# Performance work log

Hardware: AMD Instinct MI355X
Metric: run time of the kernel (lower is better)

Reference implementation:

```python
import jax, jax.numpy as jnp
import numpy as np

N = 50000
IN_C, HID_C, OUT_C = 128, 256, 128
E = 800000


def sage_conv(x, edge_index, W_l, b_l, W_r, num_nodes):
    # PyG SAGEConv (aggr='mean'): out = lin_l(mean_{j in N(i)} x_j) + lin_r(x_i)
    src, dst = edge_index[0], edge_index[1]
    msgs = x[src]  # [E, C] gather of source features
    agg = jax.ops.segment_sum(msgs, dst, num_segments=num_nodes)  # [N, C]
    deg = jax.ops.segment_sum(jnp.ones((edge_index.shape[1],), x.dtype), dst,
                              num_segments=num_nodes)
    mean = agg / jnp.maximum(deg, 1.0)[:, None]
    return mean @ W_l.T + b_l + x @ W_r.T


def setup_inputs() -> dict:
    key = jax.random.key(0)
    ks = jax.random.split(key, 8)
    x = jax.random.normal(ks[0], (N, IN_C), dtype=jnp.float32)
    edge_index = jax.random.randint(ks[1], (2, E), 0, N, dtype=jnp.int64)
    s1 = 1.0 / np.sqrt(IN_C)
    s2 = 1.0 / np.sqrt(HID_C)
    W1_l = jax.random.uniform(ks[2], (HID_C, IN_C), jnp.float32, -s1, s1)
    W1_r = jax.random.uniform(ks[3], (HID_C, IN_C), jnp.float32, -s1, s1)
    b1 = jnp.zeros((HID_C,), jnp.float32)
    W2_l = jax.random.uniform(ks[4], (OUT_C, HID_C), jnp.float32, -s2, s2)
    W2_r = jax.random.uniform(ks[5], (OUT_C, HID_C), jnp.float32, -s2, s2)
    b2 = jnp.zeros((OUT_C,), jnp.float32)
    return {"x": x, "edge_index": edge_index,
            "W1_l": W1_l, "b1": b1, "W1_r": W1_r,
            "W2_l": W2_l, "b2": b2, "W2_r": W2_r}


def reference(x, edge_index, W1_l, b1, W1_r, W2_l, b2, W2_r):
    h = sage_conv(x, edge_index, W1_l, b1, W1_r, N)
    h = jax.nn.relu(h)
    # dropout p=0.5 is identity in eval mode (inference reference)
    out = sage_conv(h, edge_index, W2_l, b2, W2_r, N)
    return out
```

## Files before the change

kernel.cpp:

```cpp
#include <hip/hip_runtime.h>

#define NN   50000
#define INC  128
#define HIDC 256
#define OUTC 128
#define NE   800000
#define MP   50048
#define CAP  64

#define EPB 4096
#define NCH ((NE + EPB - 1) / EPB)
#define RSZ 6250

typedef short bfrag __attribute__((ext_vector_type(8)));
typedef float f32x4 __attribute__((ext_vector_type(4)));
typedef unsigned short us8 __attribute__((ext_vector_type(8)));

__device__ inline unsigned short f2b(float f) {
    union { float f; unsigned u; } v; v.f = f;
    unsigned u = v.u;
    return (unsigned short)((u + 0x7fffu + ((u >> 16) & 1u)) >> 16);
}
__device__ inline float b2f(unsigned short s) {
    union { unsigned u; float f; } v; v.u = ((unsigned)s) << 16;
    return v.f;
}

__global__ __launch_bounds__(256) void k_prep(
    const float* __restrict__ x, const float* __restrict__ W1l,
    const float* __restrict__ W1r, const float* __restrict__ W2l,
    const float* __restrict__ W2r, unsigned short* __restrict__ xb16,
    unsigned short* __restrict__ A1f, unsigned short* __restrict__ B1f,
    unsigned short* __restrict__ B2f, int* __restrict__ cnt) {
    const int b = blockIdx.x;
    if (b < 3125) {
        int t = b * 256 + threadIdx.x;
        int i = t >> 4;
        int c8 = t & 15;
        const float* src = x + (size_t)i * INC + c8 * 8;
        float4 v0 = *(const float4*)src;
        float4 v1 = *(const float4*)(src + 4);
        us8 o = { f2b(v0.x), f2b(v0.y), f2b(v0.z), f2b(v0.w),
                  f2b(v1.x), f2b(v1.y), f2b(v1.z), f2b(v1.w) };
        *(us8*)(xb16 + (size_t)i * INC + c8 * 8) = o;
        size_t off = (size_t)(i >> 4) * 4096 + (size_t)(4 + (c8 >> 2)) * 512
                   + (size_t)(c8 & 3) * 128 + (size_t)(i & 15) * 8;
        *(us8*)(A1f + off) = o;
    } else if (b < 3157) {
        int t = (b - 3125) * 256 + threadIdx.x;
        int n = t >> 5;
        int k8 = t & 31;
        int k = k8 * 8;
        const float* src = (k < 128) ? (W1l + (size_t)n * INC + k)
                                     : (W1r + (size_t)n * INC + (k - 128));
        float4 v0 = *(const float4*)src;
        float4 v1 = *(const float4*)(src + 4);
        us8 o = { f2b(v0.x), f2b(v0.y), f2b(v0.z), f2b(v0.w),
                  f2b(v1.x), f2b(v1.y), f2b(v1.z), f2b(v1.w) };
        size_t off = (size_t)(n >> 4) * 4096 + (size_t)(k8 >> 2) * 512
                   + (size_t)(k8 & 3) * 128 + (size_t)(n & 15) * 8;
        *(us8*)(B1f + off) = o;
    } else if (b < 3189) {
        int t = (b - 3157) * 256 + threadIdx.x;
        int n = t >> 5;
        int k8 = t & 31;
        const float* src = (n < 128) ? (W2l + (size_t)n * HIDC + k8 * 8)
                                     : (W2r + (size_t)(n - 128) * HIDC + k8 * 8);
        float4 v0 = *(const float4*)src;
        float4 v1 = *(const float4*)(src + 4);
        us8 o = { f2b(v0.x), f2b(v0.y), f2b(v0.z), f2b(v0.w),
                  f2b(v1.x), f2b(v1.y), f2b(v1.z), f2b(v1.w) };
        size_t off = (size_t)(n >> 4) * 4096 + (size_t)(k8 >> 2) * 512
                   + (size_t)(k8 & 3) * 128 + (size_t)(n & 15) * 8;
        *(us8*)(B2f + off) = o;
    } else {
        int t = (b - 3189) * 256 + threadIdx.x;
        if (t < (NN + 3) / 4) *(int4*)(cnt + t * 4) = make_int4(0, 0, 0, 0);
    }
}

__global__ __launch_bounds__(256) void k_fill(const int* __restrict__ ei,
                                              int* __restrict__ cnt,
                                              unsigned short* __restrict__ csr) {
    const int r = blockIdx.x & 7;
    const int c = blockIdx.x >> 3;
    const int lo = r * RSZ, hi = lo + RSZ;
    const int base = c * EPB + threadIdx.x;
#pragma unroll
    for (int i = 0; i < EPB / 256; ++i) {
        int e = base + i * 256;
        if (e < NE) {
            int dst = ei[NE + e];
            if (dst >= lo && dst < hi) {
                int old = atomicAdd(&cnt[dst], 1);
                if (old < CAP) csr[dst * CAP + old] = (unsigned short)ei[e];
            }
        }
    }
}

__global__ __launch_bounds__(256) void k_gather_mean(
    const int* __restrict__ cnt, const unsigned short* __restrict__ csr,
    const unsigned short* __restrict__ xb16, unsigned short* __restrict__ A1f) {
    const int node = blockIdx.x * 4 + (threadIdx.x >> 6);
    const int lane = threadIdx.x & 63;
    const int sub = lane >> 4;
    const int cl = lane & 15;
    const int cn = cnt[node];
    const int m = (cn < CAP) ? cn : CAP;
    const unsigned short* cb = csr + node * CAP;
    float acc[8] = {};
    const unsigned short* xb = xb16 + cl * 8;
    int i = sub;
    for (; i + 4 < m; i += 8) {
        int s0 = cb[i], s1 = cb[i + 4];
        us8 v0 = *(const us8*)(xb + (size_t)s0 * INC);
        us8 v1 = *(const us8*)(xb + (size_t)s1 * INC);
#pragma unroll
        for (int j = 0; j < 8; ++j) acc[j] += b2f(v0[j]) + b2f(v1[j]);
    }
    if (i < m) {
        int s0 = cb[i];
        us8 v0 = *(const us8*)(xb + (size_t)s0 * INC);
#pragma unroll
        for (int j = 0; j < 8; ++j) acc[j] += b2f(v0[j]);
    }
#pragma unroll
    for (int j = 0; j < 8; ++j) {
        acc[j] += __shfl_xor(acc[j], 16, 64);
        acc[j] += __shfl_xor(acc[j], 32, 64);
    }
    if (sub == 0) {
        float inv = 1.0f / fmaxf((float)cn, 1.0f);
        us8 o;
#pragma unroll
        for (int j = 0; j < 8; ++j) o[j] = f2b(acc[j] * inv);
        size_t off = (size_t)(node >> 4) * 4096 + (size_t)(cl >> 2) * 512
                   + (size_t)(cl & 3) * 128 + (size_t)(node & 15) * 8;
        *(us8*)(A1f + off) = o;
    }
}

__global__ __launch_bounds__(256) void k_mgemm1(
    const unsigned short* __restrict__ A, const unsigned short* __restrict__ B,
    const float* __restrict__ bias, unsigned short* __restrict__ H) {
    __shared__ unsigned short Asl[4096];
    __shared__ unsigned short Bsl[4096];
    const int tid = threadIdx.x;
    const int lane = tid & 63;
    const int w = tid >> 6;
    const int wr = w >> 1, wc = w & 1;
    const int col = lane & 15, quad = lane >> 4;
    const int bx = blockIdx.x, by = blockIdx.y;

    f32x4 acc[4][4];
#pragma unroll
    for (int i = 0; i < 4; ++i)
#pragma unroll
        for (int j = 0; j < 4; ++j) acc[i][j] = (f32x4){0.f, 0.f, 0.f, 0.f};

    const int c0 = tid, c1 = tid + 256;
    for (int kc = 0; kc < 8; ++kc) {
        const unsigned short* Ag = A + (size_t)(bx * 8) * 4096 + kc * 512;
        const unsigned short* Bg = B + (size_t)(by * 8) * 4096 + kc * 512;
        __syncthreads();
        *(us8*)(Asl + c0 * 8) = *(const us8*)(Ag + (size_t)(c0 >> 6) * 4096 + (c0 & 63) * 8);
        *(us8*)(Asl + c1 * 8) = *(const us8*)(Ag + (size_t)(c1 >> 6) * 4096 + (c1 & 63) * 8);
        *(us8*)(Bsl + c0 * 8) = *(const us8*)(Bg + (size_t)(c0 >> 6) * 4096 + (c0 & 63) * 8);
        *(us8*)(Bsl + c1 * 8) = *(const us8*)(Bg + (size_t)(c1 >> 6) * 4096 + (c1 & 63) * 8);
        __syncthreads();
        bfrag a[4], b[4];
#pragma unroll
        for (int mt = 0; mt < 4; ++mt)
            a[mt] = *(const bfrag*)(Asl + (wr * 4 + mt) * 512 + quad * 128 + col * 8);
#pragma unroll
        for (int nt = 0; nt < 4; ++nt)
            b[nt] = *(const bfrag*)(Bsl + (wc * 4 + nt) * 512 + quad * 128 + col * 8);
#pragma unroll
        for (int mt = 0; mt < 4; ++mt)
#pragma unroll
            for (int nt = 0; nt < 4; ++nt)
                acc[mt][nt] = __builtin_amdgcn_mfma_f32_16x16x32_bf16(a[mt], b[nt], acc[mt][nt], 0, 0, 0);
    }
#pragma unroll
    for (int mt = 0; mt < 4; ++mt)
#pragma unroll
        for (int nt = 0; nt < 4; ++nt) {
            int n = by * 128 + wc * 64 + nt * 16 + col;
            float bb = bias[n];
#pragma unroll
            for (int r = 0; r < 4; ++r) {
                int m = bx * 128 + wr * 64 + mt * 16 + quad * 4 + r;
                if (m < NN) {
                    size_t off = (size_t)(m >> 4) * 4096 + (size_t)(n >> 5) * 512
                               + (size_t)((n >> 3) & 3) * 128 + (size_t)(m & 15) * 8 + (n & 7);
                    H[off] = f2b(fmaxf(acc[mt][nt][r] + bb, 0.f));
                }
            }
        }
}

__global__ __launch_bounds__(256) void k_mgemm2(
    const unsigned short* __restrict__ A, const unsigned short* __restrict__ B,
    const float* __restrict__ bias, unsigned short* __restrict__ HP,
    float* __restrict__ OUT) {
    __shared__ unsigned short Asl[4096];
    __shared__ unsigned short Bsl[4096];
    const int tid = threadIdx.x;
    const int lane = tid & 63;
    const int w = tid >> 6;
    const int wr = w >> 1, wc = w & 1;
    const int col = lane & 15, quad = lane >> 4;
    const int bx = blockIdx.x, by = blockIdx.y;

    f32x4 acc[4][4];
#pragma unroll
    for (int i = 0; i < 4; ++i)
#pragma unroll
        for (int j = 0; j < 4; ++j) acc[i][j] = (f32x4){0.f, 0.f, 0.f, 0.f};

    const int c0 = tid, c1 = tid + 256;
    for (int kc = 0; kc < 8; ++kc) {
        const unsigned short* Ag = A + (size_t)(bx * 8) * 4096 + kc * 512;
        const unsigned short* Bg = B + (size_t)(by * 8) * 4096 + kc * 512;
        __syncthreads();
        *(us8*)(Asl + c0 * 8) = *(const us8*)(Ag + (size_t)(c0 >> 6) * 4096 + (c0 & 63) * 8);
        *(us8*)(Asl + c1 * 8) = *(const us8*)(Ag + (size_t)(c1 >> 6) * 4096 + (c1 & 63) * 8);
        *(us8*)(Bsl + c0 * 8) = *(const us8*)(Bg + (size_t)(c0 >> 6) * 4096 + (c0 & 63) * 8);
        *(us8*)(Bsl + c1 * 8) = *(const us8*)(Bg + (size_t)(c1 >> 6) * 4096 + (c1 & 63) * 8);
        __syncthreads();
        bfrag a[4], b[4];
#pragma unroll
        for (int mt = 0; mt < 4; ++mt)
            a[mt] = *(const bfrag*)(Asl + (wr * 4 + mt) * 512 + quad * 128 + col * 8);
#pragma unroll
        for (int nt = 0; nt < 4; ++nt)
            b[nt] = *(const bfrag*)(Bsl + (wc * 4 + nt) * 512 + quad * 128 + col * 8);
#pragma unroll
        for (int mt = 0; mt < 4; ++mt)
#pragma unroll
            for (int nt = 0; nt < 4; ++nt)
                acc[mt][nt] = __builtin_amdgcn_mfma_f32_16x16x32_bf16(a[mt], b[nt], acc[mt][nt], 0, 0, 0);
    }
    if (by == 0) {
#pragma unroll
        for (int mt = 0; mt < 4; ++mt)
#pragma unroll
            for (int nt = 0; nt < 4; ++nt) {
                int n = wc * 64 + nt * 16 + col;
#pragma unroll
                for (int r = 0; r < 4; ++r) {
                    int m = bx * 128 + wr * 64 + mt * 16 + quad * 4 + r;
                    if (m < NN) HP[(size_t)m * OUTC + n] = f2b(acc[mt][nt][r]);
                }
            }
    } else {
#pragma unroll
        for (int mt = 0; mt < 4; ++mt)
#pragma unroll
            for (int nt = 0; nt < 4; ++nt) {
                int n = wc * 64 + nt * 16 + col;
                float bb = bias[n];
#pragma unroll
                for (int r = 0; r < 4; ++r) {
                    int m = bx * 128 + wr * 64 + mt * 16 + quad * 4 + r;
                    if (m < NN) OUT[(size_t)m * OUTC + n] = acc[mt][nt][r] + bb;
                }
            }
    }
}

__global__ __launch_bounds__(256) void k_gather_add(
    const int* __restrict__ cnt, const unsigned short* __restrict__ csr,
    const unsigned short* __restrict__ hp, float* __restrict__ out) {
    const int node = blockIdx.x * 4 + (threadIdx.x >> 6);
    const int lane = threadIdx.x & 63;
    const int sub = lane >> 4;
    const int cl = lane & 15;
    const int cn = cnt[node];
    const int m = (cn < CAP) ? cn : CAP;
    const unsigned short* cb = csr + node * CAP;
    float acc[8] = {};
    const unsigned short* hb = hp + cl * 8;
    int i = sub;
    for (; i + 4 < m; i += 8) {
        int s0 = cb[i], s1 = cb[i + 4];
        us8 v0 = *(const us8*)(hb + (size_t)s0 * OUTC);
        us8 v1 = *(const us8*)(hb + (size_t)s1 * OUTC);
#pragma unroll
        for (int j = 0; j < 8; ++j) acc[j] += b2f(v0[j]) + b2f(v1[j]);
    }
    if (i < m) {
        int s0 = cb[i];
        us8 v0 = *(const us8*)(hb + (size_t)s0 * OUTC);
#pragma unroll
        for (int j = 0; j < 8; ++j) acc[j] += b2f(v0[j]);
    }
#pragma unroll
    for (int j = 0; j < 8; ++j) {
        acc[j] += __shfl_xor(acc[j], 16, 64);
        acc[j] += __shfl_xor(acc[j], 32, 64);
    }
    if (sub == 0) {
        float inv = 1.0f / fmaxf((float)cn, 1.0f);
        float* p = out + (size_t)node * OUTC + cl * 8;
        float4 c0v = *(float4*)p;
        float4 c1v = *(float4*)(p + 4);
        c0v.x += acc[0] * inv; c0v.y += acc[1] * inv;
        c0v.z += acc[2] * inv; c0v.w += acc[3] * inv;
        c1v.x += acc[4] * inv; c1v.y += acc[5] * inv;
        c1v.z += acc[6] * inv; c1v.w += acc[7] * inv;
        *(float4*)p = c0v;
        *(float4*)(p + 4) = c1v;
    }
}

extern "C" void kernel_launch(void* const* d_in, const int* in_sizes, int n_in,
                              void* d_out, int out_size, void* d_ws, size_t ws_size,
                              hipStream_t stream) {
    const float* x   = (const float*)d_in[0];
    const int*   ei  = (const int*)d_in[1];
    const float* W1l = (const float*)d_in[2];
    const float* b1  = (const float*)d_in[3];
    const float* W1r = (const float*)d_in[4];
    const float* W2l = (const float*)d_in[5];
    const float* b2  = (const float*)d_in[6];
    const float* W2r = (const float*)d_in[7];
    float* out = (float*)d_out;

    int* cnt = (int*)d_ws;
    unsigned short* csr = (unsigned short*)(cnt + ((NN + 63) & ~63));
    unsigned short* A1f  = csr + (size_t)NN * CAP;
    unsigned short* Hf   = A1f + (size_t)MP * 256;
    unsigned short* xb16 = Hf + (size_t)MP * 256;
    unsigned short* hp   = xb16 + (size_t)NN * 128;
    unsigned short* B1f  = hp + (size_t)NN * 128;
    unsigned short* B2f  = B1f + 256 * 256;

    k_prep<<<3238, 256, 0, stream>>>(x, W1l, W1r, W2l, W2r, xb16, A1f, B1f, B2f, cnt);
    k_fill<<<NCH * 8, 256, 0, stream>>>(ei, cnt, csr);
    k_gather_mean<<<NN / 4, 256, 0, stream>>>(cnt, csr, xb16, A1f);

    dim3 g(MP / 128, 2);
    k_mgemm1<<<g, 256, 0, stream>>>(A1f, B1f, b1, Hf);
    k_mgemm2<<<g, 256, 0, stream>>>(Hf, B2f, b2, hp, out);

    k_gather_add<<<NN / 4, 256, 0, stream>>>(cnt, csr, hp, out);
}
```

Baseline: 247.3 us.

## Fuse the two dense GEMMs into one kernel keeping hidden tile in LDS

Merges the layer-1 GEMM (with bias and ReLU) and the layer-2 GEMM into a single kernel. Each block loads a 64-row A tile into shared memory once, writes the hidden activations back into the same LDS buffer, and runs the second GEMM from there. This removes the global round trip of the 50k x 256 hidden matrix and one kernel launch. B fragments are now read directly from global memory rather than staged through LDS, and there are fewer, larger blocks using 32KB of LDS each, which may lower occupancy.

New measurement: 227.9 us. 7.9% less time.

```diff
diff --git a/kernel.cpp b/kernel.cpp
--- a/kernel.cpp
+++ b/kernel.cpp
@@ -141,116 +141,93 @@
     }
 }
 
-__global__ __launch_bounds__(256) void k_mgemm1(
-    const unsigned short* __restrict__ A, const unsigned short* __restrict__ B,
-    const float* __restrict__ bias, unsigned short* __restrict__ H) {
-    __shared__ unsigned short Asl[4096];
-    __shared__ unsigned short Bsl[4096];
+__global__ __launch_bounds__(256) void k_mgemm_fused(
+    const unsigned short* __restrict__ A, const unsigned short* __restrict__ B1,
+    const float* __restrict__ b1, const unsigned short* __restrict__ B2,
+    const float* __restrict__ b2, unsigned short* __restrict__ HP,
+    float* __restrict__ OUT) {
+    __shared__ unsigned short Hsl[16384];
     const int tid = threadIdx.x;
     const int lane = tid & 63;
     const int w = tid >> 6;
-    const int wr = w >> 1, wc = w & 1;
     const int col = lane & 15, quad = lane >> 4;
-    const int bx = blockIdx.x, by = blockIdx.y;
+    const int m0 = blockIdx.x * 64;
+
+    {
+        const us8* src = (const us8*)(A + (size_t)(m0 >> 4) * 4096);
+        us8* dst = (us8*)Hsl;
+#pragma unroll
+        for (int i = 0; i < 8; ++i) dst[tid + i * 256] = src[tid + i * 256];
+    }
+    __syncthreads();
 
     f32x4 acc[4][4];
 #pragma unroll
     for (int i = 0; i < 4; ++i)
 #pragma unroll
         for (int j = 0; j < 4; ++j) acc[i][j] = (f32x4){0.f, 0.f, 0.f, 0.f};
-
-    const int c0 = tid, c1 = tid + 256;
+#pragma unroll
     for (int kc = 0; kc < 8; ++kc) {
-        const unsigned short* Ag = A + (size_t)(bx * 8) * 4096 + kc * 512;
-        const unsigned short* Bg = B + (size_t)(by * 8) * 4096 + kc * 512;
-        __syncthreads();
-        *(us8*)(Asl + c0 * 8) = *(const us8*)(Ag + (size_t)(c0 >> 6) * 4096 + (c0 & 63) * 8);
-        *(us8*)(Asl + c1 * 8) = *(const us8*)(Ag + (size_t)(c1 >> 6) * 4096 + (c1 & 63) * 8);
-        *(us8*)(Bsl + c0 * 8) = *(const us8*)(Bg + (size_t)(c0 >> 6) * 4096 + (c0 & 63) * 8);
-        *(us8*)(Bsl + c1 * 8) = *(const us8*)(Bg + (size_t)(c1 >> 6) * 4096 + (c1 & 63) * 8);
-        __syncthreads();
         bfrag a[4], b[4];
 #pragma unroll
         for (int mt = 0; mt < 4; ++mt)
-            a[mt] = *(const bfrag*)(Asl + (wr * 4 + mt) * 512 + quad * 128 + col * 8);
+            a[mt] = *(const bfrag*)(Hsl + mt * 4096 + kc * 512 + quad * 128 + col * 8);
 #pragma unroll
         for (int nt = 0; nt < 4; ++nt)
-            b[nt] = *(const bfrag*)(Bsl + (wc * 4 + nt) * 512 + quad * 128 + col * 8);
+            b[nt] = *(const bfrag*)(B1 + (size_t)(w * 4 + nt) * 4096 + kc * 512 + quad * 128 + col * 8);
 #pragma unroll
         for (int mt = 0; mt < 4; ++mt)
 #pragma unroll
             for (int nt = 0; nt < 4; ++nt)
                 acc[mt][nt] = __builtin_amdgcn_mfma_f32_16x16x32_bf16(a[mt], b[nt], acc[mt][nt], 0, 0, 0);
     }
-#pragma unroll
-    for (int mt = 0; mt < 4; ++mt)
-#pragma unroll
-        for (int nt = 0; nt < 4; ++nt) {
-            int n = by * 128 + wc * 64 + nt * 16 + col;
-            float bb = bias[n];
+    __syncthreads();
+
+#pragma unroll
+    for (int nt = 0; nt < 4; ++nt) {
+        int n = w * 64 + nt * 16 + col;
+        float bb = b1[n];
+        int noff = (n >> 5) * 512 + ((n >> 3) & 3) * 128 + (n & 7);
+#pragma unroll
+        for (int mt = 0; mt < 4; ++mt) {
 #pragma unroll
             for (int r = 0; r < 4; ++r) {
-                int m = bx * 128 + wr * 64 + mt * 16 + quad * 4 + r;
-                if (m < NN) {
-                    size_t off = (size_t)(m >> 4) * 4096 + (size_t)(n >> 5) * 512
-                               + (size_t)((n >> 3) & 3) * 128 + (size_t)(m & 15) * 8 + (n & 7);
-                    H[off] = f2b(fmaxf(acc[mt][nt][r] + bb, 0.f));
-                }
+                int ml = quad * 4 + r;
+                Hsl[mt * 4096 + noff + ml * 8] = f2b(fmaxf(acc[mt][nt][r] + bb, 0.f));
             }
         }
-}
-
-__global__ __launch_bounds__(256) void k_mgemm2(
-    const unsigned short* __restrict__ A, const unsigned short* __restrict__ B,
-    const float* __restrict__ bias, unsigned short* __restrict__ HP,
-    float* __restrict__ OUT) {
-    __shared__ unsigned short Asl[4096];
-    __shared__ unsigned short Bsl[4096];
-    const int tid = threadIdx.x;
-    const int lane = tid & 63;
-    const int w = tid >> 6;
-    const int wr = w >> 1, wc = w & 1;
-    const int col = lane & 15, quad = lane >> 4;
-    const int bx = blockIdx.x, by = blockIdx.y;
-
-    f32x4 acc[4][4];
+    }
+    __syncthreads();
+
 #pragma unroll
     for (int i = 0; i < 4; ++i)
 #pragma unroll
         for (int j = 0; j < 4; ++j) acc[i][j] = (f32x4){0.f, 0.f, 0.f, 0.f};
-
-    const int c0 = tid, c1 = tid + 256;
+#pragma unroll
     for (int kc = 0; kc < 8; ++kc) {
-        const unsigned short* Ag = A + (size_t)(bx * 8) * 4096 + kc * 512;
-        const unsigned short* Bg = B + (size_t)(by * 8) * 4096 + kc * 512;
-        __syncthreads();
-        *(us8*)(Asl + c0 * 8) = *(const us8*)(Ag + (size_t)(c0 >> 6) * 4096 + (c0 & 63) * 8);
-        *(us8*)(Asl + c1 * 8) = *(const us8*)(Ag + (size_t)(c1 >> 6) * 4096 + (c1 & 63) * 8);
-        *(us8*)(Bsl + c0 * 8) = *(const us8*)(Bg + (size_t)(c0 >> 6) * 4096 + (c0 & 63) * 8);
-        *(us8*)(Bsl + c1 * 8) = *(const us8*)(Bg + (size_t)(c1 >> 6) * 4096 + (c1 & 63) * 8);
-        __syncthreads();
         bfrag a[4], b[4];
 #pragma unroll
         for (int mt = 0; mt < 4; ++mt)
-            a[mt] = *(const bfrag*)(Asl + (wr * 4 + mt) * 512 + quad * 128 + col * 8);
+            a[mt] = *(const bfrag*)(Hsl + mt * 4096 + kc * 512 + quad * 128 + col * 8);
 #pragma unroll
         for (int nt = 0; nt < 4; ++nt)
-            b[nt] = *(const bfrag*)(Bsl + (wc * 4 + nt) * 512 + quad * 128 + col * 8);
+            b[nt] = *(const bfrag*)(B2 + (size_t)(w * 4 + nt) * 4096 + kc * 512 + quad * 128 + col * 8);
 #pragma unroll
         for (int mt = 0; mt < 4; ++mt)
 #pragma unroll
             for (int nt = 0; nt < 4; ++nt)
                 acc[mt][nt] = __builtin_amdgcn_mfma_f32_16x16x32_bf16(a[mt], b[nt], acc[mt][nt], 0, 0, 0);
     }
-    if (by == 0) {
+
+    if (w < 2) {
 #pragma unroll
         for (int mt = 0; mt < 4; ++mt)
 #pragma unroll
             for (int nt = 0; nt < 4; ++nt) {
-                int n = wc * 64 + nt * 16 + col;
+                int n = w * 64 + nt * 16 + col;
 #pragma unroll
                 for (int r = 0; r < 4; ++r) {
-                    int m = bx * 128 + wr * 64 + mt * 16 + quad * 4 + r;
+                    int m = m0 + mt * 16 + quad * 4 + r;
                     if (m < NN) HP[(size_t)m * OUTC + n] = f2b(acc[mt][nt][r]);
                 }
             }
@@ -259,11 +236,11 @@
         for (int mt = 0; mt < 4; ++mt)
 #pragma unroll
             for (int nt = 0; nt < 4; ++nt) {
-                int n = wc * 64 + nt * 16 + col;
-                float bb = bias[n];
+                int n = (w - 2) * 64 + nt * 16 + col;
+                float bb = b2[n];
 #pragma unroll
                 for (int r = 0; r < 4; ++r) {
-                    int m = bx * 128 + wr * 64 + mt * 16 + quad * 4 + r;
+                    int m = m0 + mt * 16 + quad * 4 + r;
                     if (m < NN) OUT[(size_t)m * OUTC + n] = acc[mt][nt][r] + bb;
                 }
             }
@@ -331,8 +308,7 @@
     int* cnt = (int*)d_ws;
     unsigned short* csr = (unsigned short*)(cnt + ((NN + 63) & ~63));
     unsigned short* A1f  = csr + (size_t)NN * CAP;
-    unsigned short* Hf   = A1f + (size_t)MP * 256;
-    unsigned short* xb16 = Hf + (size_t)MP * 256;
+    unsigned short* xb16 = A1f + (size_t)MP * 256;
     unsigned short* hp   = xb16 + (size_t)NN * 128;
     unsigned short* B1f  = hp + (size_t)NN * 128;
     unsigned short* B2f  = B1f + 256 * 256;
@@ -341,9 +317,7 @@
     k_fill<<<NCH * 8, 256, 0, stream>>>(ei, cnt, csr);
     k_gather_mean<<<NN / 4, 256, 0, stream>>>(cnt, csr, xb16, A1f);
 
-    dim3 g(MP / 128, 2);
-    k_mgemm1<<<g, 256, 0, stream>>>(A1f, B1f, b1, Hf);
-    k_mgemm2<<<g, 256, 0, stream>>>(Hf, B2f, b2, hp, out);
+    k_mgemm_fused<<<MP / 64, 256, 0, stream>>>(A1f, B1f, b1, B2f, b2, hp, out);
 
     k_gather_add<<<NN / 4, 256, 0, stream>>>(cnt, csr, hp, out);
 }
```
